# Kernel tuning notes

Hardware: AMD Instinct MI355X
Metric: run time of the kernel (lower is better)

The kernel has to match this reference:

```python
import jax, jax.numpy as jnp
import numpy as np

EPS = 1e-5

def _bn2d(x, g, b, m, v):
    s = (1, -1, 1, 1)
    return (x - m.reshape(s)) * (g.reshape(s) * jax.lax.rsqrt(v.reshape(s) + EPS)) + b.reshape(s)

def _bn1d(x, g, b, m, v):
    return (x - m) * (g * jax.lax.rsqrt(v + EPS)) + b

def _conv3x3(x, w, b):
    y = jax.lax.conv_general_dilated(x, w, (1, 1), ((1, 1), (1, 1)),
                                     dimension_numbers=('NCHW', 'OIHW', 'NCHW'))
    return y + b.reshape(1, -1, 1, 1)

def setup_inputs() -> dict:
    key = jax.random.key(0)
    ks = iter(jax.random.split(key, 64))
    B = 512
    d = {}
    d['anchor'] = jax.random.normal(next(ks), (B, 1, 16, 8), jnp.float32)
    d['positive'] = jax.random.normal(next(ks), (B, 1, 16, 8), jnp.float32)
    d['negative'] = jax.random.normal(next(ks), (B, 1, 16, 8), jnp.float32)

    def bn_params(c):
        g = jax.random.normal(next(ks), (c,), jnp.float32) * 0.1 + 1.0
        b = jax.random.normal(next(ks), (c,), jnp.float32) * 0.1
        m = jax.random.normal(next(ks), (c,), jnp.float32) * 0.1
        v = jax.random.uniform(next(ks), (c,), jnp.float32, 0.5, 1.5)
        return g, b, m, v

    d['bn0_g'], d['bn0_b'], d['bn0_m'], d['bn0_v'] = bn_params(1)
    d['conv1_w'] = jax.random.normal(next(ks), (64, 1, 3, 3), jnp.float32) * 0.1
    d['conv1_b'] = jax.random.normal(next(ks), (64,), jnp.float32) * 0.1
    d['bn1_g'], d['bn1_b'], d['bn1_m'], d['bn1_v'] = bn_params(64)
    d['conv2_w'] = jax.random.normal(next(ks), (64, 64, 3, 3), jnp.float32) * 0.04
    d['conv2_b'] = jax.random.normal(next(ks), (64,), jnp.float32) * 0.1
    d['bn2_g'], d['bn2_b'], d['bn2_m'], d['bn2_v'] = bn_params(64)
    # locally-connected: kernel_size=1 -> per-position unshared channel mix (o,c,h,w)
    d['lc1_w'] = jax.random.normal(next(ks), (64, 64, 16, 8), jnp.float32) * 0.125
    d['bn3_g'], d['bn3_b'], d['bn3_m'], d['bn3_v'] = bn_params(64)
    d['lc2_w'] = jax.random.normal(next(ks), (64, 64, 16, 8), jnp.float32) * 0.125
    d['bn4_g'], d['bn4_b'], d['bn4_m'], d['bn4_v'] = bn_params(64)
    d['fc1_w'] = jax.random.normal(next(ks), (512, 8192), jnp.float32) * 0.01
    d['fc1_b'] = jax.random.normal(next(ks), (512,), jnp.float32) * 0.1
    d['bnf1_g'], d['bnf1_b'], d['bnf1_m'], d['bnf1_v'] = bn_params(512)
    d['fc2_w'] = jax.random.normal(next(ks), (512, 512), jnp.float32) * 0.04
    d['fc2_b'] = jax.random.normal(next(ks), (512,), jnp.float32) * 0.1
    d['bnf2_g'], d['bnf2_b'], d['bnf2_m'], d['bnf2_v'] = bn_params(512)
    d['fc3_w'] = jax.random.normal(next(ks), (128, 512), jnp.float32) * 0.04
    d['fc3_b'] = jax.random.normal(next(ks), (128,), jnp.float32) * 0.1
    d['bnf3_g'], d['bnf3_b'], d['bnf3_m'], d['bnf3_v'] = bn_params(128)
    d['out_w'] = jax.random.normal(next(ks), (128, 128), jnp.float32) * 0.09
    d['out_b'] = jax.random.normal(next(ks), (128,), jnp.float32) * 0.1
    return d

def _embedding(x, p):
    x = _bn2d(x, p['bn0_g'], p['bn0_b'], p['bn0_m'], p['bn0_v'])
    x = _conv3x3(x, p['conv1_w'], p['conv1_b'])
    x = jax.nn.relu(_bn2d(x, p['bn1_g'], p['bn1_b'], p['bn1_m'], p['bn1_v']))
    x = _conv3x3(x, p['conv2_w'], p['conv2_b'])
    x = jax.nn.relu(_bn2d(x, p['bn2_g'], p['bn2_b'], p['bn2_m'], p['bn2_v']))
    # locally connected (kernel 1): per-position channel mix, no huge unfold intermediate
    x = jnp.einsum('bchw,ochw->bohw', x, p['lc1_w'])
    x = jax.nn.relu(_bn2d(x, p['bn3_g'], p['bn3_b'], p['bn3_m'], p['bn3_v']))
    x = jnp.einsum('bchw,ochw->bohw', x, p['lc2_w'])
    x = jax.nn.relu(_bn2d(x, p['bn4_g'], p['bn4_b'], p['bn4_m'], p['bn4_v']))
    # dropout is identity in eval mode
    x = x.reshape(x.shape[0], -1)  # (B, 8192)
    x = x @ p['fc1_w'].T + p['fc1_b']
    x = jax.nn.relu(_bn1d(x, p['bnf1_g'], p['bnf1_b'], p['bnf1_m'], p['bnf1_v']))
    x = x @ p['fc2_w'].T + p['fc2_b']
    x = jax.nn.relu(_bn1d(x, p['bnf2_g'], p['bnf2_b'], p['bnf2_m'], p['bnf2_v']))
    x = x @ p['fc3_w'].T + p['fc3_b']
    x = jax.nn.relu(_bn1d(x, p['bnf3_g'], p['bnf3_b'], p['bnf3_m'], p['bnf3_v']))
    return x @ p['out_w'].T + p['out_b']

def reference(anchor, positive, negative,
              bn0_g, bn0_b, bn0_m, bn0_v,
              conv1_w, conv1_b, bn1_g, bn1_b, bn1_m, bn1_v,
              conv2_w, conv2_b, bn2_g, bn2_b, bn2_m, bn2_v,
              lc1_w, bn3_g, bn3_b, bn3_m, bn3_v,
              lc2_w, bn4_g, bn4_b, bn4_m, bn4_v,
              fc1_w, fc1_b, bnf1_g, bnf1_b, bnf1_m, bnf1_v,
              fc2_w, fc2_b, bnf2_g, bnf2_b, bnf2_m, bnf2_v,
              fc3_w, fc3_b, bnf3_g, bnf3_b, bnf3_m, bnf3_v,
              out_w, out_b):
    p = dict(bn0_g=bn0_g, bn0_b=bn0_b, bn0_m=bn0_m, bn0_v=bn0_v,
             conv1_w=conv1_w, conv1_b=conv1_b, bn1_g=bn1_g, bn1_b=bn1_b, bn1_m=bn1_m, bn1_v=bn1_v,
             conv2_w=conv2_w, conv2_b=conv2_b, bn2_g=bn2_g, bn2_b=bn2_b, bn2_m=bn2_m, bn2_v=bn2_v,
             lc1_w=lc1_w, bn3_g=bn3_g, bn3_b=bn3_b, bn3_m=bn3_m, bn3_v=bn3_v,
             lc2_w=lc2_w, bn4_g=bn4_g, bn4_b=bn4_b, bn4_m=bn4_m, bn4_v=bn4_v,
             fc1_w=fc1_w, fc1_b=fc1_b, bnf1_g=bnf1_g, bnf1_b=bnf1_b, bnf1_m=bnf1_m, bnf1_v=bnf1_v,
             fc2_w=fc2_w, fc2_b=fc2_b, bnf2_g=bnf2_g, bnf2_b=bnf2_b, bnf2_m=bnf2_m, bnf2_v=bnf2_v,
             fc3_w=fc3_w, fc3_b=fc3_b, bnf3_g=bnf3_g, bnf3_b=bnf3_b, bnf3_m=bnf3_m, bnf3_v=bnf3_v,
             out_w=out_w, out_b=out_b)
    return (_embedding(anchor, p), _embedding(positive, p), _embedding(negative, p))
```

## Files before the change

### kernel.cpp

```cpp
#include <hip/hip_runtime.h>
#include <math.h>

#define EPS 1e-5f
#define FD 8192

typedef __attribute__((ext_vector_type(8))) __bf16 bf16x8;
typedef __attribute__((ext_vector_type(4))) float f32x4;

static __device__ __forceinline__ f32x4 mfma16(bf16x8 a, bf16x8 b, f32x4 c) {
    return __builtin_amdgcn_mfma_f32_16x16x32_bf16(a, b, c, 0, 0, 0);
}

__global__ __launch_bounds__(256) void k_conv_mega(
    const float* __restrict__ inA, const float* __restrict__ inP, const float* __restrict__ inN,
    const float* __restrict__ bn0g, const float* __restrict__ bn0b,
    const float* __restrict__ bn0m, const float* __restrict__ bn0v,
    const float* __restrict__ w1, const float* __restrict__ b1,
    const float* __restrict__ bn1g, const float* __restrict__ bn1b,
    const float* __restrict__ bn1m, const float* __restrict__ bn1v,
    const float* __restrict__ w2, const float* __restrict__ b2,
    const float* __restrict__ bn2g, const float* __restrict__ bn2b,
    const float* __restrict__ bn2m, const float* __restrict__ bn2v,
    __bf16* __restrict__ act,
    const float* __restrict__ lc1, const float* __restrict__ lc2,
    const float* __restrict__ fc1w, const float* __restrict__ fc2w,
    const float* __restrict__ fc3w, const float* __restrict__ outw,
    __bf16* __restrict__ lc1frag, __bf16* __restrict__ lc2frag,
    __bf16* __restrict__ fc1Wb, __bf16* __restrict__ wf23) {
    const int bb = blockIdx.x;
    const int t = threadIdx.x;
    __shared__ __align__(16) char smem[43136];

    if (bb >= 1536) {
        const int pb = bb - 1536;
        float (*wbuf)[130] = (float(*)[130])smem;
        if (pb < 128) {
            const int layer = pb >> 6, o = pb & 63;
            const int wo = o >> 4, lo = o & 15;
            const float* src = (layer ? lc2 : lc1) + (size_t)o * 8192;
            __bf16* dst = layer ? lc2frag : lc1frag;
#pragma unroll
            for (int pass = 0; pass < 8; ++pass) {
                int i = pass * 1024 + t * 4;
                float4 v = *(const float4*)(src + i);
                int c = i >> 7, p = i & 127;
                wbuf[c][p + 0] = v.x; wbuf[c][p + 1] = v.y;
                wbuf[c][p + 2] = v.z; wbuf[c][p + 3] = v.w;
            }
            __syncthreads();
#pragma unroll
            for (int pass = 0; pass < 4; ++pass) {
                int slot = pass * 256 + t;
                int p = slot >> 3, chunk = (slot >> 2) & 1, q = slot & 3;
                bf16x8 v;
#pragma unroll
                for (int j = 0; j < 8; ++j)
                    v[j] = (__bf16)wbuf[chunk * 32 + q * 8 + j][p];
                *(bf16x8*)(dst + ((size_t)((p * 2 + chunk) * 4 + wo) * 64 + q * 16 + lo) * 8) = v;
            }
        } else if (pb < 640) {
            const int n = pb - 128;
            const float* src = fc1w + (size_t)n * 8192;
            __bf16* dst = fc1Wb + (size_t)n * 8192;
#pragma unroll
            for (int pass = 0; pass < 8; ++pass) {
                int i = pass * 1024 + t * 4;
                float4 v = *(const float4*)(src + i);
                int c = i >> 7, p = i & 127;
                wbuf[c][p + 0] = v.x; wbuf[c][p + 1] = v.y;
                wbuf[c][p + 2] = v.z; wbuf[c][p + 3] = v.w;
            }
            __syncthreads();
#pragma unroll
            for (int pass = 0; pass < 16; ++pass) {
                int kA = (pass * 256 + t) * 2;
                int c = kA & 63, p = kA >> 6;
                __bf16 tmp[2];
                tmp[0] = (__bf16)wbuf[c][p];
                tmp[1] = (__bf16)wbuf[c + 1][p];
                *(unsigned int*)(dst + kA) = *(unsigned int*)tmp;
            }
        } else {
            int i = (pb - 640) * 256 + t;
            float v;
            if (i < 262144) v = fc2w[i];
            else if (i < 327680) v = fc3w[i - 262144];
            else v = outw[i - 327680];
            wf23[i] = (__bf16)v;
        }
        return;
    }

    const int b = bb;
    const int lane = t & 63, w = t >> 6;
    const int q = lane >> 4, li = lane & 15;
    const int n0 = w * 16;
    const int o = n0 + li;
    const float* src = (b < 512 ? inA : (b < 1024 ? inP : inN)) + (size_t)(b & 511) * 128;

    float* xpad = (float*)smem;
    __bf16* A1 = (__bf16*)(smem + 768);
    __bf16* Xp = (__bf16*)(smem + 11008);
    float* s1 = (float*)(smem + 42112);
    float* sh1 = (float*)(smem + 42368);
    float* s2 = (float*)(smem + 42624);
    float* sh2 = (float*)(smem + 42880);

    bf16x8 w1f;
#pragma unroll
    for (int j = 0; j < 8; ++j) {
        int k = q * 8 + j;
        w1f[j] = (k < 9) ? (__bf16)w1[o * 9 + k] : (__bf16)0.0f;
    }

    {
        int* xz = (int*)Xp;
        for (int i = t; i < 7776; i += 256) xz[i] = 0;
        if (t < 180) xpad[t] = 0.f;
        if (t < 64) {
            float sa = bn1g[t] * rsqrtf(bn1v[t] + EPS);
            s1[t] = sa;
            sh1[t] = (b1[t] - bn1m[t]) * sa + bn1b[t];
            float sb = bn2g[t] * rsqrtf(bn2v[t] + EPS);
            s2[t] = sb;
            sh2[t] = (b2[t] - bn2m[t]) * sb + bn2b[t];
        }
    }
    __syncthreads();
    if (t < 128) {
        float s0 = bn0g[0] * rsqrtf(bn0v[0] + EPS);
        float v = (src[t] - bn0m[0]) * s0 + bn0b[0];
        xpad[((t >> 3) + 1) * 10 + (t & 7) + 1] = v;
    }
    __syncthreads();
    {
        int p = t >> 1, half = t & 1;
        int r = p >> 3, cl = p & 7;
        bf16x8 v0, v1;
#pragma unroll
        for (int jj = 0; jj < 8; ++jj) {
            int j = half * 16 + jj;
            v0[jj] = (j < 9) ? (__bf16)xpad[(r + j / 3) * 10 + cl + (j % 3)] : (__bf16)0.f;
            int j2 = half * 16 + 8 + jj;
            v1[jj] = (j2 < 9) ? (__bf16)xpad[(r + j2 / 3) * 10 + cl + (j2 % 3)] : (__bf16)0.f;
        }
        *(bf16x8*)&A1[p * 40 + half * 16] = v0;
        *(bf16x8*)&A1[p * 40 + half * 16 + 8] = v1;
    }
    __syncthreads();
    {
        const float sco = s1[o], sho = sh1[o];
#pragma unroll
        for (int m = 0; m < 8; ++m) {
            bf16x8 a = *(const bf16x8*)&A1[(m * 16 + li) * 40 + q * 8];
            f32x4 z = {0.f, 0.f, 0.f, 0.f};
            f32x4 d = mfma16(a, w1f, z);
#pragma unroll
            for (int r = 0; r < 4; ++r) {
                int p = m * 16 + q * 4 + r;
                float v = fmaxf(d[r] * sco + sho, 0.f);
                Xp[(((p >> 3) + 1) * 12 + (p & 7) + 1) * 72 + o] = (__bf16)v;
            }
        }
    }
    __syncthreads();
    f32x4 accA[4], accB[4];
#pragma unroll
    for (int i = 0; i < 4; ++i) {
        accA[i] = (f32x4){0.f, 0.f, 0.f, 0.f};
        accB[i] = (f32x4){0.f, 0.f, 0.f, 0.f};
    }
    const int cl2 = li & 7;
#pragma unroll
    for (int ch = 0; ch < 2; ++ch) {
        bf16x8 wf[9];
        const int cbase = ch * 32 + q * 8;
#pragma unroll
        for (int tap = 0; tap < 9; ++tap)
#pragma unroll
            for (int j = 0; j < 8; ++j)
                wf[tap][j] = (__bf16)w2[(size_t)o * 576 + (cbase + j) * 9 + tap];
#pragma unroll
        for (int mp = 0; mp < 4; ++mp) {
            const int r0 = mp * 4 + (li >> 3);
            const int base0 = (r0 * 12 + cl2) * 72 + q * 8 + ch * 32;
            const int base1 = base0 + 1728;
#pragma unroll
            for (int tap = 0; tap < 9; ++tap) {
                const int tofs = ((tap / 3) * 12 + (tap % 3)) * 72;
                bf16x8 a0 = *(const bf16x8*)&Xp[base0 + tofs];
                bf16x8 a1 = *(const bf16x8*)&Xp[base1 + tofs];
                accA[mp] = mfma16(a0, wf[tap], accA[mp]);
                accB[mp] = mfma16(a1, wf[tap], accB[mp]);
            }
        }
    }
    __syncthreads();
    {
        const float sco = s2[o], sho = sh2[o];
#pragma unroll
        for (int mp = 0; mp < 4; ++mp) {
#pragma unroll
            for (int r = 0; r < 4; ++r) {
                int p0 = mp * 32 + q * 4 + r;
                Xp[p0 * 72 + o] = (__bf16)fmaxf(accA[mp][r] * sco + sho, 0.f);
                Xp[(p0 + 16) * 72 + o] = (__bf16)fmaxf(accB[mp][r] * sco + sho, 0.f);
            }
        }
    }
    __syncthreads();
    {
        int p = t >> 1, half = t & 1;
        const __bf16* rp = Xp + p * 72 + half * 32;
        __bf16* ob = act + (size_t)b * FD + p * 64 + half * 32;
        *(bf16x8*)ob = *(const bf16x8*)rp;
        *(bf16x8*)(ob + 8) = *(const bf16x8*)(rp + 8);
        *(bf16x8*)(ob + 16) = *(const bf16x8*)(rp + 16);
        *(bf16x8*)(ob + 24) = *(const bf16x8*)(rp + 24);
    }
}

__global__ __launch_bounds__(256) void k_lc_mfma(
    const __bf16* __restrict__ lc1frag, const __bf16* __restrict__ lc2frag,
    const float* __restrict__ bn3g, const float* __restrict__ bn3b,
    const float* __restrict__ bn3m, const float* __restrict__ bn3v,
    const float* __restrict__ bn4g, const float* __restrict__ bn4b,
    const float* __restrict__ bn4m, const float* __restrict__ bn4v,
    __bf16* __restrict__ act) {
    const int p = blockIdx.x;
    const int b0 = blockIdx.y * 128;
    const int t = threadIdx.x;
    const int lane = t & 63, w = t >> 6;
    const int q = lane >> 4, li = lane & 15;
    const int n0 = w * 16;

    __shared__ __align__(16) __bf16 xs[128 * 72];
    __shared__ __align__(16) __bf16 ys[128 * 72];
    __shared__ float s3[64], sh3[64], s4[64], sh4[64];

    if (t < 64) {
        float sa = bn3g[t] * rsqrtf(bn3v[t] + EPS);
        s3[t] = sa; sh3[t] = bn3b[t] - bn3m[t] * sa;
        float sb = bn4g[t] * rsqrtf(bn4v[t] + EPS);
        s4[t] = sb; sh4[t] = bn4b[t] - bn4m[t] * sb;
    }
    {
        int s = t >> 1, half = t & 1;
        const __bf16* rp = act + (size_t)(b0 + s) * FD + p * 64 + half * 32;
        __bf16* xp = xs + s * 72 + half * 32;
        *(bf16x8*)xp = *(const bf16x8*)rp;
        *(bf16x8*)(xp + 8) = *(const bf16x8*)(rp + 8);
        *(bf16x8*)(xp + 16) = *(const bf16x8*)(rp + 16);
        *(bf16x8*)(xp + 24) = *(const bf16x8*)(rp + 24);
    }
    bf16x8 w1a = *(const bf16x8*)(lc1frag + ((size_t)((p * 2 + 0) * 4 + w) * 64 + lane) * 8);
    bf16x8 w1b = *(const bf16x8*)(lc1frag + ((size_t)((p * 2 + 1) * 4 + w) * 64 + lane) * 8);
    bf16x8 w2a = *(const bf16x8*)(lc2frag + ((size_t)((p * 2 + 0) * 4 + w) * 64 + lane) * 8);
    bf16x8 w2b = *(const bf16x8*)(lc2frag + ((size_t)((p * 2 + 1) * 4 + w) * 64 + lane) * 8);
    __syncthreads();
    {
        const float sco = s3[n0 + li], sho = sh3[n0 + li];
#pragma unroll
        for (int m = 0; m < 8; ++m) {
            bf16x8 a0 = *(const bf16x8*)&xs[(m * 16 + li) * 72 + q * 8];
            bf16x8 a1 = *(const bf16x8*)&xs[(m * 16 + li) * 72 + 32 + q * 8];
            f32x4 acc = {0.f, 0.f, 0.f, 0.f};
            acc = mfma16(a0, w1a, acc);
            acc = mfma16(a1, w1b, acc);
#pragma unroll
            for (int r = 0; r < 4; ++r) {
                int bl = m * 16 + q * 4 + r;
                ys[bl * 72 + n0 + li] = (__bf16)fmaxf(acc[r] * sco + sho, 0.f);
            }
        }
    }
    __syncthreads();
    {
        const float sco = s4[n0 + li], sho = sh4[n0 + li];
#pragma unroll
        for (int m = 0; m < 8; ++m) {
            bf16x8 a0 = *(const bf16x8*)&ys[(m * 16 + li) * 72 + q * 8];
            bf16x8 a1 = *(const bf16x8*)&ys[(m * 16 + li) * 72 + 32 + q * 8];
            f32x4 acc = {0.f, 0.f, 0.f, 0.f};
            acc = mfma16(a0, w2a, acc);
            acc = mfma16(a1, w2b, acc);
#pragma unroll
            for (int r = 0; r < 4; ++r) {
                int bl = m * 16 + q * 4 + r;
                xs[bl * 72 + n0 + li] = (__bf16)fmaxf(acc[r] * sco + sho, 0.f);
            }
        }
    }
    __syncthreads();
    {
        int s = t >> 1, half = t & 1;
        const __bf16* rp = xs + s * 72 + half * 32;
        __bf16* ob = act + (size_t)(b0 + s) * FD + p * 64 + half * 32;
        *(bf16x8*)ob = *(const bf16x8*)rp;
        *(bf16x8*)(ob + 8) = *(const bf16x8*)(rp + 8);
        *(bf16x8*)(ob + 16) = *(const bf16x8*)(rp + 16);
        *(bf16x8*)(ob + 24) = *(const bf16x8*)(rp + 24);
    }
}

__global__ __launch_bounds__(256) void k_fc1_mfma(
    const __bf16* __restrict__ A, const __bf16* __restrict__ Wb,
    float* __restrict__ part) {
    const int t = threadIdx.x;
    const int lane = t & 63, w = t >> 6;
    const int q = lane >> 4, li = lane & 15;
    const int m0 = blockIdx.x * 64, n0 = blockIdx.y * 64;
    const int k0 = blockIdx.z * 2048;
    const int wm = (w & 1) * 32, wn = (w >> 1) * 32;

    __shared__ __align__(16) __bf16 As[64 * 72];
    __shared__ __align__(16) __bf16 Bs[64 * 72];

    f32x4 acc[2][2];
#pragma unroll
    for (int i = 0; i < 2; ++i)
#pragma unroll
        for (int j = 0; j < 2; ++j) acc[i][j] = (f32x4){0.f, 0.f, 0.f, 0.f};

    const int row = t >> 2, qt = t & 3;
    const __bf16* Ag = A + (size_t)(m0 + row) * 8192 + k0 + qt * 16;
    const __bf16* Bg = Wb + (size_t)(n0 + row) * 8192 + k0 + qt * 16;

    bf16x8 pa0 = *(const bf16x8*)Ag;
    bf16x8 pa1 = *(const bf16x8*)(Ag + 8);
    bf16x8 pb0 = *(const bf16x8*)Bg;
    bf16x8 pb1 = *(const bf16x8*)(Bg + 8);

    for (int step = 0; step < 32; ++step) {
        *(bf16x8*)&As[row * 72 + qt * 16] = pa0;
        *(bf16x8*)&As[row * 72 + qt * 16 + 8] = pa1;
        *(bf16x8*)&Bs[row * 72 + qt * 16] = pb0;
        *(bf16x8*)&Bs[row * 72 + qt * 16 + 8] = pb1;
        __syncthreads();
        Ag += 64; Bg += 64;
        if (step < 31) {
            pa0 = *(const bf16x8*)Ag;
            pa1 = *(const bf16x8*)(Ag + 8);
            pb0 = *(const bf16x8*)Bg;
            pb1 = *(const bf16x8*)(Bg + 8);
        }
#pragma unroll
        for (int kc = 0; kc < 2; ++kc) {
            bf16x8 af[2], bfr[2];
#pragma unroll
            for (int i = 0; i < 2; ++i)
                af[i] = *(const bf16x8*)&As[(wm + i * 16 + li) * 72 + kc * 32 + q * 8];
#pragma unroll
            for (int j = 0; j < 2; ++j)
                bfr[j] = *(const bf16x8*)&Bs[(wn + j * 16 + li) * 72 + kc * 32 + q * 8];
#pragma unroll
            for (int i = 0; i < 2; ++i)
#pragma unroll
                for (int j = 0; j < 2; ++j)
                    acc[i][j] = mfma16(af[i], bfr[j], acc[i][j]);
        }
        __syncthreads();
    }
    float* pp = part + (size_t)blockIdx.z * 786432;
#pragma unroll
    for (int i = 0; i < 2; ++i) {
#pragma unroll
        for (int r = 0; r < 4; ++r) {
            int m = m0 + wm + i * 16 + q * 4 + r;
#pragma unroll
            for (int j = 0; j < 2; ++j) {
                int n = n0 + wn + j * 16 + li;
                pp[(size_t)m * 512 + n] = acc[i][j][r];
            }
        }
    }
}

__global__ __launch_bounds__(256) void k_fc2_mfma(
    const float* __restrict__ part,
    const float* __restrict__ b1f,
    const float* __restrict__ g1, const float* __restrict__ bb1,
    const float* __restrict__ m1, const float* __restrict__ v1,
    const __bf16* __restrict__ W2, const float* __restrict__ b2f,
    const float* __restrict__ g2, const float* __restrict__ bb2,
    const float* __restrict__ m2, const float* __restrict__ v2,
    __bf16* __restrict__ out) {
    const int t = threadIdx.x;
    const int lane = t & 63, w = t >> 6;
    const int q = lane >> 4, li = lane & 15;
    const int m0 = blockIdx.x * 64, n0 = blockIdx.y * 64;
    const int wm = (w & 1) * 32, wn = (w >> 1) * 32;

    __shared__ __align__(16) __bf16 Ared[64 * 520];
    __shared__ float esc[512], ehh[512];

    for (int n = t; n < 512; n += 256) {
        float s = g1[n] * rsqrtf(v1[n] + EPS);
        esc[n] = s;
        ehh[n] = (b1f[n] - m1[n]) * s + bb1[n];
    }
    __syncthreads();
    {
        const int row = t >> 2, seg = t & 3;
#pragma unroll
        for (int j = 0; j < 32; ++j) {
            int k4 = seg + j * 4;
            size_t off = (size_t)(m0 + row) * 512 + k4 * 4;
            float4 s0 = *(const float4*)(part + off);
            float4 s1 = *(const float4*)(part + 786432 + off);
            float4 s2 = *(const float4*)(part + 2 * 786432 + off);
            float4 s3 = *(const float4*)(part + 3 * 786432 + off);
            float v[4] = {s0.x + s1.x + s2.x + s3.x, s0.y + s1.y + s2.y + s3.y,
                          s0.z + s1.z + s2.z + s3.z, s0.w + s1.w + s2.w + s3.w};
            __bf16 o4[4];
#pragma unroll
            for (int jj = 0; jj < 4; ++jj) {
                int k = k4 * 4 + jj;
                o4[jj] = (__bf16)fmaxf(v[jj] * esc[k] + ehh[k], 0.f);
            }
            *(uint2*)&Ared[row * 520 + k4 * 4] = *(uint2*)o4;
        }
    }
    __syncthreads();
    f32x4 acc[2][2];
#pragma unroll
    for (int i = 0; i < 2; ++i)
#pragma unroll
        for (int j = 0; j < 2; ++j) acc[i][j] = (f32x4){0.f, 0.f, 0.f, 0.f};
    for (int k0 = 0; k0 < 512; k0 += 32) {
        bf16x8 af[2], bfr[2];
#pragma unroll
        for (int j = 0; j < 2; ++j) {
            int n = n0 + wn + j * 16 + li;
            bfr[j] = *(const bf16x8*)(W2 + (size_t)n * 512 + k0 + q * 8);
        }
#pragma unroll
        for (int i = 0; i < 2; ++i)
            af[i] = *(const bf16x8*)&Ared[(wm + i * 16 + li) * 520 + k0 + q * 8];
#pragma unroll
        for (int i = 0; i < 2; ++i)
#pragma unroll
            for (int j = 0; j < 2; ++j)
                acc[i][j] = mfma16(af[i], bfr[j], acc[i][j]);
    }
    float bi[2], sc[2], hh[2];
#pragma unroll
    for (int j = 0; j < 2; ++j) {
        int n = n0 + wn + j * 16 + li;
        bi[j] = b2f[n];
        sc[j] = g2[n] * rsqrtf(v2[n] + EPS);
        hh[j] = bb2[n] - m2[n] * sc[j];
    }
#pragma unroll
    for (int i = 0; i < 2; ++i) {
#pragma unroll
        for (int r = 0; r < 4; ++r) {
            int m = m0 + wm + i * 16 + q * 4 + r;
#pragma unroll
            for (int j = 0; j < 2; ++j) {
                int n = n0 + wn + j * 16 + li;
                float x = (acc[i][j][r] + bi[j]) * sc[j] + hh[j];
                out[(size_t)m * 512 + n] = (__bf16)fmaxf(x, 0.f);
            }
        }
    }
}

__global__ __launch_bounds__(256) void k_fc3out(
    const __bf16* __restrict__ A, const __bf16* __restrict__ W3,
    const __bf16* __restrict__ Wo,
    const float* __restrict__ b3,
    const float* __restrict__ bng, const float* __restrict__ bnb,
    const float* __restrict__ bnm, const float* __restrict__ bnv,
    const float* __restrict__ bo, float* __restrict__ out) {
    const int t = threadIdx.x;
    const int lane = t & 63, w = t >> 6;
    const int q = lane >> 4, li = lane & 15;
    const int m0 = blockIdx.x * 32;
    const int wn = w * 32;

    __shared__ __align__(16) __bf16 y3[32 * 136];

    f32x4 acc[2][2];
#pragma unroll
    for (int i = 0; i < 2; ++i)
#pragma unroll
        for (int j = 0; j < 2; ++j) acc[i][j] = (f32x4){0.f, 0.f, 0.f, 0.f};
    for (int k0 = 0; k0 < 512; k0 += 32) {
        bf16x8 af[2], bfr[2];
#pragma unroll
        for (int i = 0; i < 2; ++i)
            af[i] = *(const bf16x8*)(A + (size_t)(m0 + i * 16 + li) * 512 + k0 + q * 8);
#pragma unroll
        for (int j = 0; j < 2; ++j) {
            int n = wn + j * 16 + li;
            bfr[j] = *(const bf16x8*)(W3 + (size_t)n * 512 + k0 + q * 8);
        }
#pragma unroll
        for (int i = 0; i < 2; ++i)
#pragma unroll
            for (int j = 0; j < 2; ++j)
                acc[i][j] = mfma16(af[i], bfr[j], acc[i][j]);
    }
#pragma unroll
    for (int j = 0; j < 2; ++j) {
        int n = wn + j * 16 + li;
        float sc = bng[n] * rsqrtf(bnv[n] + EPS);
        float hh = bnb[n] - bnm[n] * sc;
        float bi = b3[n];
#pragma unroll
        for (int i = 0; i < 2; ++i)
#pragma unroll
            for (int r = 0; r < 4; ++r) {
                int m = i * 16 + q * 4 + r;
                float x = (acc[i][j][r] + bi) * sc + hh;
                y3[m * 136 + n] = (__bf16)fmaxf(x, 0.f);
            }
    }
    __syncthreads();
    f32x4 acc2[2][2];
#pragma unroll
    for (int i = 0; i < 2; ++i)
#pragma unroll
        for (int j = 0; j < 2; ++j) acc2[i][j] = (f32x4){0.f, 0.f, 0.f, 0.f};
#pragma unroll
    for (int step = 0; step < 4; ++step) {
        const int k0 = step * 32;
        bf16x8 af[2], bfr[2];
#pragma unroll
        for (int i = 0; i < 2; ++i)
            af[i] = *(const bf16x8*)&y3[(i * 16 + li) * 136 + k0 + q * 8];
#pragma unroll
        for (int j = 0; j < 2; ++j) {
            int n = wn + j * 16 + li;
            bfr[j] = *(const bf16x8*)(Wo + (size_t)n * 128 + k0 + q * 8);
        }
#pragma unroll
        for (int i = 0; i < 2; ++i)
#pragma unroll
            for (int j = 0; j < 2; ++j)
                acc2[i][j] = mfma16(af[i], bfr[j], acc2[i][j]);
    }
#pragma unroll
    for (int j = 0; j < 2; ++j) {
        int n = wn + j * 16 + li;
        float bi = bo[n];
#pragma unroll
        for (int i = 0; i < 2; ++i)
#pragma unroll
            for (int r = 0; r < 4; ++r) {
                int m = m0 + i * 16 + q * 4 + r;
                out[(size_t)m * 128 + n] = acc2[i][j][r] + bi;
            }
    }
}

extern "C" void kernel_launch(void* const* d_in, const int* in_sizes, int n_in,
                              void* d_out, int out_size, void* d_ws, size_t ws_size,
                              hipStream_t stream) {
    const float* inA    = (const float*)d_in[0];
    const float* inP    = (const float*)d_in[1];
    const float* inN    = (const float*)d_in[2];
    const float* bn0g   = (const float*)d_in[3];
    const float* bn0b   = (const float*)d_in[4];
    const float* bn0m   = (const float*)d_in[5];
    const float* bn0v   = (const float*)d_in[6];
    const float* conv1w = (const float*)d_in[7];
    const float* conv1b = (const float*)d_in[8];
    const float* bn1g   = (const float*)d_in[9];
    const float* bn1b   = (const float*)d_in[10];
    const float* bn1m   = (const float*)d_in[11];
    const float* bn1v   = (const float*)d_in[12];
    const float* conv2w = (const float*)d_in[13];
    const float* conv2b = (const float*)d_in[14];
    const float* bn2g   = (const float*)d_in[15];
    const float* bn2b   = (const float*)d_in[16];
    const float* bn2m   = (const float*)d_in[17];
    const float* bn2v   = (const float*)d_in[18];
    const float* lc1w   = (const float*)d_in[19];
    const float* bn3g   = (const float*)d_in[20];
    const float* bn3b   = (const float*)d_in[21];
    const float* bn3m   = (const float*)d_in[22];
    const float* bn3v   = (const float*)d_in[23];
    const float* lc2w   = (const float*)d_in[24];
    const float* bn4g   = (const float*)d_in[25];
    const float* bn4b   = (const float*)d_in[26];
    const float* bn4m   = (const float*)d_in[27];
    const float* bn4v   = (const float*)d_in[28];
    const float* fc1w   = (const float*)d_in[29];
    const float* fc1b   = (const float*)d_in[30];
    const float* bnf1g  = (const float*)d_in[31];
    const float* bnf1b  = (const float*)d_in[32];
    const float* bnf1m  = (const float*)d_in[33];
    const float* bnf1v  = (const float*)d_in[34];
    const float* fc2w   = (const float*)d_in[35];
    const float* fc2b   = (const float*)d_in[36];
    const float* bnf2g  = (const float*)d_in[37];
    const float* bnf2b  = (const float*)d_in[38];
    const float* bnf2m  = (const float*)d_in[39];
    const float* bnf2v  = (const float*)d_in[40];
    const float* fc3w   = (const float*)d_in[41];
    const float* fc3b   = (const float*)d_in[42];
    const float* bnf3g  = (const float*)d_in[43];
    const float* bnf3b  = (const float*)d_in[44];
    const float* bnf3m  = (const float*)d_in[45];
    const float* bnf3v  = (const float*)d_in[46];
    const float* outw   = (const float*)d_in[47];
    const float* outb   = (const float*)d_in[48];

    char* wsb = (char*)d_ws;
    __bf16* lc1frag = (__bf16*)wsb;
    __bf16* lc2frag = lc1frag + 524288;
    __bf16* fc1Wb   = lc2frag + 524288;
    __bf16* wf23    = fc1Wb + 4194304;
    __bf16* act     = wf23 + 344064;
    __bf16* act4    = act + 12582912;
    float*  part    = (float*)(((uintptr_t)(act4 + 786432) + 15) & ~(uintptr_t)15);
    __bf16* wf2 = wf23;
    __bf16* wf3 = wf23 + 262144;
    __bf16* wfo = wf23 + 327680;

    k_conv_mega<<<3520, 256, 0, stream>>>(inA, inP, inN,
        bn0g, bn0b, bn0m, bn0v, conv1w, conv1b, bn1g, bn1b, bn1m, bn1v,
        conv2w, conv2b, bn2g, bn2b, bn2m, bn2v, act,
        lc1w, lc2w, fc1w, fc2w, fc3w, outw,
        lc1frag, lc2frag, fc1Wb, wf23);

    k_lc_mfma<<<dim3(128, 12), 256, 0, stream>>>(lc1frag, lc2frag,
        bn3g, bn3b, bn3m, bn3v, bn4g, bn4b, bn4m, bn4v, act);

    k_fc1_mfma<<<dim3(24, 8, 4), 256, 0, stream>>>(act, fc1Wb, part);

    k_fc2_mfma<<<dim3(24, 8), 256, 0, stream>>>(part,
        fc1b, bnf1g, bnf1b, bnf1m, bnf1v,
        wf2, fc2b, bnf2g, bnf2b, bnf2m, bnf2v, act4);

    k_fc3out<<<48, 256, 0, stream>>>(act4, wf3, wfo, fc3b,
        bnf3g, bnf3b, bnf3m, bnf3v, outb, (float*)d_out);
}
```

Baseline: 269.4 us.

## Prepack conv weight fragments, enlarge fc1 tiles, and restructure fc2 reduction

Adds a small prep kernel that converts conv1/conv2 weights into bf16 MFMA fragment layout once. The conv kernel then loads prepacked fragments with vector loads instead of doing per-block strided fp32 gathers. fc1 moves from 64x64 to 128x128 tiles with an 8-way K split, giving more reuse per block. fc2 now gives each block 32 rows across all 512 columns and reduces 8 partial buffers. Costs are an extra launch, more fc1 registers and partial-sum traffic, and fewer fc2 blocks.

```diff
diff --git a/kernel.cpp b/kernel.cpp
--- a/kernel.cpp
+++ b/kernel.cpp
@@ -9,16 +9,48 @@
 
 static __device__ __forceinline__ f32x4 mfma16(bf16x8 a, bf16x8 b, f32x4 c) {
     return __builtin_amdgcn_mfma_f32_16x16x32_bf16(a, b, c, 0, 0, 0);
+}
+
+__global__ __launch_bounds__(256) void k_prep_frags(
+    const float* __restrict__ w1, const float* __restrict__ w2,
+    __bf16* __restrict__ w1frag, __bf16* __restrict__ w2frag) {
+    const int bb = blockIdx.x, t = threadIdx.x;
+    if (bb == 0) {
+        const int lane = t & 63, w = t >> 6;
+        const int q = lane >> 4, li = lane & 15;
+        const int o = w * 16 + li;
+        bf16x8 v;
+#pragma unroll
+        for (int j = 0; j < 8; ++j) {
+            int k = q * 8 + j;
+            v[j] = (k < 9) ? (__bf16)w1[o * 9 + k] : (__bf16)0.0f;
+        }
+        *(bf16x8*)(w1frag + t * 8) = v;
+    } else {
+        const int id = (bb - 1) * 256 + t;
+        const int lane = id & 63;
+        const int w = (id >> 6) & 3;
+        const int chunk = (id >> 8) & 1;
+        const int tap = id >> 9;
+        const int q = lane >> 4, li = lane & 15;
+        const int o = w * 16 + li;
+        const int c0 = chunk * 32 + q * 8;
+        bf16x8 v;
+#pragma unroll
+        for (int j = 0; j < 8; ++j)
+            v[j] = (__bf16)w2[(o * 64 + c0 + j) * 9 + tap];
+        *(bf16x8*)(w2frag + (size_t)id * 8) = v;
+    }
 }
 
 __global__ __launch_bounds__(256) void k_conv_mega(
     const float* __restrict__ inA, const float* __restrict__ inP, const float* __restrict__ inN,
     const float* __restrict__ bn0g, const float* __restrict__ bn0b,
     const float* __restrict__ bn0m, const float* __restrict__ bn0v,
-    const float* __restrict__ w1, const float* __restrict__ b1,
+    const __bf16* __restrict__ w1frag, const float* __restrict__ b1,
     const float* __restrict__ bn1g, const float* __restrict__ bn1b,
     const float* __restrict__ bn1m, const float* __restrict__ bn1v,
-    const float* __restrict__ w2, const float* __restrict__ b2,
+    const __bf16* __restrict__ w2frag, const float* __restrict__ b2,
     const float* __restrict__ bn2g, const float* __restrict__ bn2b,
     const float* __restrict__ bn2m, const float* __restrict__ bn2v,
     __bf16* __restrict__ act,
@@ -106,12 +138,14 @@
     float* s2 = (float*)(smem + 42624);
     float* sh2 = (float*)(smem + 42880);
 
-    bf16x8 w1f;
-#pragma unroll
-    for (int j = 0; j < 8; ++j) {
-        int k = q * 8 + j;
-        w1f[j] = (k < 9) ? (__bf16)w1[o * 9 + k] : (__bf16)0.0f;
-    }
+    bf16x8 w1f = *(const bf16x8*)(w1frag + (size_t)(w * 64 + lane) * 8);
+    bf16x8 w2f[18];
+#pragma unroll
+    for (int tap = 0; tap < 9; ++tap)
+#pragma unroll
+        for (int ch = 0; ch < 2; ++ch)
+            w2f[tap * 2 + ch] = *(const bf16x8*)(w2frag +
+                ((size_t)((tap * 2 + ch) * 4 + w) * 64 + lane) * 8);
 
     {
         int* xz = (int*)Xp;
@@ -170,28 +204,23 @@
         accA[i] = (f32x4){0.f, 0.f, 0.f, 0.f};
         accB[i] = (f32x4){0.f, 0.f, 0.f, 0.f};
     }
-    const int cl2 = li & 7;
-#pragma unroll
-    for (int ch = 0; ch < 2; ++ch) {
-        bf16x8 wf[9];
-        const int cbase = ch * 32 + q * 8;
-#pragma unroll
-        for (int tap = 0; tap < 9; ++tap)
-#pragma unroll
-            for (int j = 0; j < 8; ++j)
-                wf[tap][j] = (__bf16)w2[(size_t)o * 576 + (cbase + j) * 9 + tap];
+    {
+        const int cl = li & 7;
 #pragma unroll
         for (int mp = 0; mp < 4; ++mp) {
             const int r0 = mp * 4 + (li >> 3);
-            const int base0 = (r0 * 12 + cl2) * 72 + q * 8 + ch * 32;
+            const int base0 = (r0 * 12 + cl) * 72 + q * 8;
             const int base1 = base0 + 1728;
 #pragma unroll
             for (int tap = 0; tap < 9; ++tap) {
                 const int tofs = ((tap / 3) * 12 + (tap % 3)) * 72;
-                bf16x8 a0 = *(const bf16x8*)&Xp[base0 + tofs];
-                bf16x8 a1 = *(const bf16x8*)&Xp[base1 + tofs];
-                accA[mp] = mfma16(a0, wf[tap], accA[mp]);
-                accB[mp] = mfma16(a1, wf[tap], accB[mp]);
+#pragma unroll
+                for (int ch = 0; ch < 2; ++ch) {
+                    bf16x8 a0 = *(const bf16x8*)&Xp[base0 + tofs + ch * 32];
+                    bf16x8 a1 = *(const bf16x8*)&Xp[base1 + tofs + ch * 32];
+                    accA[mp] = mfma16(a0, w2f[tap * 2 + ch], accA[mp]);
+                    accB[mp] = mfma16(a1, w2f[tap * 2 + ch], accB[mp]);
+                }
             }
         }
     }
@@ -309,66 +338,68 @@
     const int t = threadIdx.x;
     const int lane = t & 63, w = t >> 6;
     const int q = lane >> 4, li = lane & 15;
-    const int m0 = blockIdx.x * 64, n0 = blockIdx.y * 64;
-    const int k0 = blockIdx.z * 2048;
-    const int wm = (w & 1) * 32, wn = (w >> 1) * 32;
-
-    __shared__ __align__(16) __bf16 As[64 * 72];
-    __shared__ __align__(16) __bf16 Bs[64 * 72];
-
-    f32x4 acc[2][2];
-#pragma unroll
-    for (int i = 0; i < 2; ++i)
-#pragma unroll
-        for (int j = 0; j < 2; ++j) acc[i][j] = (f32x4){0.f, 0.f, 0.f, 0.f};
-
-    const int row = t >> 2, qt = t & 3;
-    const __bf16* Ag = A + (size_t)(m0 + row) * 8192 + k0 + qt * 16;
-    const __bf16* Bg = Wb + (size_t)(n0 + row) * 8192 + k0 + qt * 16;
-
-    bf16x8 pa0 = *(const bf16x8*)Ag;
-    bf16x8 pa1 = *(const bf16x8*)(Ag + 8);
-    bf16x8 pb0 = *(const bf16x8*)Bg;
-    bf16x8 pb1 = *(const bf16x8*)(Bg + 8);
-
-    for (int step = 0; step < 32; ++step) {
-        *(bf16x8*)&As[row * 72 + qt * 16] = pa0;
-        *(bf16x8*)&As[row * 72 + qt * 16 + 8] = pa1;
-        *(bf16x8*)&Bs[row * 72 + qt * 16] = pb0;
-        *(bf16x8*)&Bs[row * 72 + qt * 16 + 8] = pb1;
+    const int m0 = blockIdx.x * 128, n0 = blockIdx.y * 128;
+    const int k0 = blockIdx.z * 1024;
+    const int wm = (w & 1) * 64, wn = (w >> 1) * 64;
+
+    __shared__ __align__(16) __bf16 As[128 * 72];
+    __shared__ __align__(16) __bf16 Bs[128 * 72];
+
+    f32x4 acc[4][4];
+#pragma unroll
+    for (int i = 0; i < 4; ++i)
+#pragma unroll
+        for (int j = 0; j < 4; ++j) acc[i][j] = (f32x4){0.f, 0.f, 0.f, 0.f};
+
+    const int row = t >> 1, half = t & 1;
+    const __bf16* Ag = A + (size_t)(m0 + row) * 8192 + k0 + half * 32;
+    const __bf16* Bg = Wb + (size_t)(n0 + row) * 8192 + k0 + half * 32;
+
+    bf16x8 pa0 = *(const bf16x8*)Ag, pa1 = *(const bf16x8*)(Ag + 8);
+    bf16x8 pa2 = *(const bf16x8*)(Ag + 16), pa3 = *(const bf16x8*)(Ag + 24);
+    bf16x8 pb0 = *(const bf16x8*)Bg, pb1 = *(const bf16x8*)(Bg + 8);
+    bf16x8 pb2 = *(const bf16x8*)(Bg + 16), pb3 = *(const bf16x8*)(Bg + 24);
+
+    for (int step = 0; step < 16; ++step) {
+        __bf16* as = &As[row * 72 + half * 32];
+        __bf16* bs = &Bs[row * 72 + half * 32];
+        *(bf16x8*)as = pa0; *(bf16x8*)(as + 8) = pa1;
+        *(bf16x8*)(as + 16) = pa2; *(bf16x8*)(as + 24) = pa3;
+        *(bf16x8*)bs = pb0; *(bf16x8*)(bs + 8) = pb1;
+        *(bf16x8*)(bs + 16) = pb2; *(bf16x8*)(bs + 24) = pb3;
         __syncthreads();
         Ag += 64; Bg += 64;
-        if (step < 31) {
-            pa0 = *(const bf16x8*)Ag;
-            pa1 = *(const bf16x8*)(Ag + 8);
-            pb0 = *(const bf16x8*)Bg;
-            pb1 = *(const bf16x8*)(Bg + 8);
+        if (step < 15) {
+            pa0 = *(const bf16x8*)Ag; pa1 = *(const bf16x8*)(Ag + 8);
+            pa2 = *(const bf16x8*)(Ag + 16); pa3 = *(const bf16x8*)(Ag + 24);
+            pb0 = *(const bf16x8*)Bg; pb1 = *(const bf16x8*)(Bg + 8);
+            pb2 = *(const bf16x8*)(Bg + 16); pb3 = *(const bf16x8*)(Bg + 24);
         }
 #pragma unroll
         for (int kc = 0; kc < 2; ++kc) {
-            bf16x8 af[2], bfr[2];
-#pragma unroll
-            for (int i = 0; i < 2; ++i)
+            bf16x8 af[4], bfr[4];
+#pragma unroll
+            for (int i = 0; i < 4; ++i)
                 af[i] = *(const bf16x8*)&As[(wm + i * 16 + li) * 72 + kc * 32 + q * 8];
 #pragma unroll
-            for (int j = 0; j < 2; ++j)
+            for (int j = 0; j < 4; ++j)
                 bfr[j] = *(const bf16x8*)&Bs[(wn + j * 16 + li) * 72 + kc * 32 + q * 8];
 #pragma unroll
-            for (int i = 0; i < 2; ++i)
-#pragma unroll
-                for (int j = 0; j < 2; ++j)
+            for (int i = 0; i < 4; ++i)
+#pragma unroll
+                for (int j = 0; j < 4; ++j)
                     acc[i][j] = mfma16(af[i], bfr[j], acc[i][j]);
         }
         __syncthreads();
     }
     float* pp = part + (size_t)blockIdx.z * 786432;
 #pragma unroll
-    for (int i = 0; i < 2; ++i) {
+    for (int i = 0; i < 4; ++i) {
 #pragma unroll
         for (int r = 0; r < 4; ++r) {
             int m = m0 + wm + i * 16 + q * 4 + r;
 #pragma unroll
-            for (int j = 0; j < 2; ++j) {
+            for (int j = 0; j < 4; ++j) {
                 int n = n0 + wn + j * 16 + li;
                 pp[(size_t)m * 512 + n] = acc[i][j][r];
             }
@@ -376,7 +407,7 @@
     }
 }
 
-__global__ __launch_bounds__(256) void k_fc2_mfma(
+__global__ __launch_bounds__(256) void k_fc2_cr(
     const float* __restrict__ part,
     const float* __restrict__ b1f,
     const float* __restrict__ g1, const float* __restrict__ bb1,
@@ -388,10 +419,9 @@
     const int t = threadIdx.x;
     const int lane = t & 63, w = t >> 6;
     const int q = lane >> 4, li = lane & 15;
-    const int m0 = blockIdx.x * 64, n0 = blockIdx.y * 64;
-    const int wm = (w & 1) * 32, wn = (w >> 1) * 32;
-
-    __shared__ __align__(16) __bf16 Ared[64 * 520];
+    const int m0 = blockIdx.x * 32;
+
+    __shared__ __align__(16) __bf16 Ared[32 * 520];
     __shared__ float esc[512], ehh[512];
 
     for (int n = t; n < 512; n += 256) {
@@ -401,68 +431,60 @@
     }
     __syncthreads();
     {
-        const int row = t >> 2, seg = t & 3;
-#pragma unroll
-        for (int j = 0; j < 32; ++j) {
-            int k4 = seg + j * 4;
+        const int row = t >> 3, seg = t & 7;
+#pragma unroll
+        for (int j = 0; j < 16; ++j) {
+            int k4 = seg * 16 + j;
             size_t off = (size_t)(m0 + row) * 512 + k4 * 4;
-            float4 s0 = *(const float4*)(part + off);
-            float4 s1 = *(const float4*)(part + 786432 + off);
-            float4 s2 = *(const float4*)(part + 2 * 786432 + off);
-            float4 s3 = *(const float4*)(part + 3 * 786432 + off);
-            float v[4] = {s0.x + s1.x + s2.x + s3.x, s0.y + s1.y + s2.y + s3.y,
-                          s0.z + s1.z + s2.z + s3.z, s0.w + s1.w + s2.w + s3.w};
+            float vx = 0.f, vy = 0.f, vz = 0.f, vw = 0.f;
+#pragma unroll
+            for (int z = 0; z < 8; ++z) {
+                float4 s = *(const float4*)(part + (size_t)z * 786432 + off);
+                vx += s.x; vy += s.y; vz += s.z; vw += s.w;
+            }
+            float vv[4] = {vx, vy, vz, vw};
             __bf16 o4[4];
 #pragma unroll
             for (int jj = 0; jj < 4; ++jj) {
                 int k = k4 * 4 + jj;
-                o4[jj] = (__bf16)fmaxf(v[jj] * esc[k] + ehh[k], 0.f);
+                o4[jj] = (__bf16)fmaxf(vv[jj] * esc[k] + ehh[k], 0.f);
             }
             *(uint2*)&Ared[row * 520 + k4 * 4] = *(uint2*)o4;
         }
     }
     __syncthreads();
-    f32x4 acc[2][2];
+    f32x4 acc[2][8];
 #pragma unroll
     for (int i = 0; i < 2; ++i)
 #pragma unroll
-        for (int j = 0; j < 2; ++j) acc[i][j] = (f32x4){0.f, 0.f, 0.f, 0.f};
+        for (int j = 0; j < 8; ++j) acc[i][j] = (f32x4){0.f, 0.f, 0.f, 0.f};
     for (int k0 = 0; k0 < 512; k0 += 32) {
-        bf16x8 af[2], bfr[2];
-#pragma unroll
-        for (int j = 0; j < 2; ++j) {
-            int n = n0 + wn + j * 16 + li;
-            bfr[j] = *(const bf16x8*)(W2 + (size_t)n * 512 + k0 + q * 8);
-        }
-#pragma unroll
-        for (int i = 0; i < 2; ++i)
-            af[i] = *(const bf16x8*)&Ared[(wm + i * 16 + li) * 520 + k0 + q * 8];
-#pragma unroll
-        for (int i = 0; i < 2; ++i)
-#pragma unroll
-            for (int j = 0; j < 2; ++j)
-                acc[i][j] = mfma16(af[i], bfr[j], acc[i][j]);
-    }
-    float bi[2], sc[2], hh[2];
-#pragma unroll
-    for (int j = 0; j < 2; ++j) {
-        int n = n0 + wn + j * 16 + li;
-        bi[j] = b2f[n];
-        sc[j] = g2[n] * rsqrtf(v2[n] + EPS);
-        hh[j] = bb2[n] - m2[n] * sc[j];
-    }
-#pragma unroll
-    for (int i = 0; i < 2; ++i) {
-#pragma unroll
-        for (int r = 0; r < 4; ++r) {
-            int m = m0 + wm + i * 16 + q * 4 + r;
-#pragma unroll
-            for (int j = 0; j < 2; ++j) {
-                int n = n0 + wn + j * 16 + li;
-                float x = (acc[i][j][r] + bi[j]) * sc[j] + hh[j];
+        bf16x8 af[2];
+#pragma unroll
+        for (int i = 0; i < 2; ++i)
+            af[i] = *(const bf16x8*)&Ared[(i * 16 + li) * 520 + k0 + q * 8];
+#pragma unroll
+        for (int j = 0; j < 8; ++j) {
+            int n = w * 128 + j * 16 + li;
+            bf16x8 bf = *(const bf16x8*)(W2 + (size_t)n * 512 + k0 + q * 8);
+#pragma unroll
+            for (int i = 0; i < 2; ++i)
+                acc[i][j] = mfma16(af[i], bf, acc[i][j]);
+        }
+    }
+#pragma unroll
+    for (int j = 0; j < 8; ++j) {
+        int n = w * 128 + j * 16 + li;
+        float sc = g2[n] * rsqrtf(v2[n] + EPS);
+        float hh = (b2f[n] - m2[n]) * sc + bb2[n];
+#pragma unroll
+        for (int i = 0; i < 2; ++i)
+#pragma unroll
+            for (int r = 0; r < 4; ++r) {
+                int m = m0 + i * 16 + q * 4 + r;
+                float x = acc[i][j][r] * sc + hh;
                 out[(size_t)m * 512 + n] = (__bf16)fmaxf(x, 0.f);
             }
-        }
     }
 }
 
@@ -609,7 +631,9 @@
     const float* outb   = (const float*)d_in[48];
 
     char* wsb = (char*)d_ws;
-    __bf16* lc1frag = (__bf16*)wsb;
+    __bf16* w1frag  = (__bf16*)wsb;
+    __bf16* w2frag  = w1frag + 2048;
+    __bf16* lc1frag = w2frag + 36864;
     __bf16* lc2frag = lc1frag + 524288;
     __bf16* fc1Wb   = lc2frag + 524288;
     __bf16* wf23    = fc1Wb + 4194304;
@@ -620,18 +644,20 @@
     __bf16* wf3 = wf23 + 262144;
     __bf16* wfo = wf23 + 327680;
 
+    k_prep_frags<<<19, 256, 0, stream>>>(conv1w, conv2w, w1frag, w2frag);
+
     k_conv_mega<<<3520, 256, 0, stream>>>(inA, inP, inN,
-        bn0g, bn0b, bn0m, bn0v, conv1w, conv1b, bn1g, bn1b, bn1m, bn1v,
-        conv2w, conv2b, bn2g, bn2b, bn2m, bn2v, act,
+        bn0g, bn0b, bn0m, bn0v, w1frag, conv1b, bn1g, bn1b, bn1m, bn1v,
+        w2frag, conv2b, bn2g, bn2b, bn2m, bn2v, act,
         lc1w, lc2w, fc1w, fc2w, fc3w, outw,
         lc1frag, lc2frag, fc1Wb, wf23);
 
     k_lc_mfma<<<dim3(128, 12), 256, 0, stream>>>(lc1frag, lc2frag,
         bn3g, bn3b, bn3m, bn3v, bn4g, bn4b, bn4m, bn4v, act);
 
-    k_fc1_mfma<<<dim3(24, 8, 4), 256, 0, stream>>>(act, fc1Wb, part);
-
-    k_fc2_mfma<<<dim3(24, 8), 256, 0, stream>>>(part,
+    k_fc1_mfma<<<dim3(12, 4, 8), 256, 0, stream>>>(act, fc1Wb, part);
+
+    k_fc2_cr<<<48, 256, 0, stream>>>(part,
         fc1b, bnf1g, bnf1b, bnf1m, bnf1v,
         wf2, fc2b, bnf2g, bnf2b, bnf2m, bnf2v, act4);
 
```

Result: slower. 287.6 us (+6.7%).
